# Kernel tuning notes

Hardware: AMD Instinct MI355X
Metric: run time of the kernel (lower is better)

The kernel has to match this reference:

```python
import jax, jax.numpy as jnp
import numpy as np

N, M, D_K, D_V = 8192, 8192, 128, 128
SCALING = 1.0 / D_K  # module uses 1/d_k, NOT 1/sqrt(d_k)


def setup_inputs() -> dict:
    key = jax.random.key(0)
    kq, kk, kv = jax.random.split(key, 3)
    Q = jax.random.normal(kq, (N, D_K), dtype=jnp.float32)
    K = jax.random.normal(kk, (M, D_K), dtype=jnp.float32)
    V = jax.random.normal(kv, (M, D_V), dtype=jnp.float32)
    return {"Q": Q, "K": K, "V": V}


def reference(Q, K, V):
    # dots = Q @ K^T * (1/d_k)  -> [N, M]
    dots = jnp.einsum("nd,md->nm", Q, K) * SCALING
    # softmax over keys; dropout p=0 is identity
    attn = jax.nn.softmax(dots, axis=-1)
    # output = attn @ V -> [N, d_v]
    return jnp.einsum("nm,mv->nv", attn, V)
```

## Files before the change

kernel.cpp:

```cpp
#include <hip/hip_runtime.h>
#include <hip/hip_bf16.h>
#include <cstdint>
#include <cstddef>


typedef __attribute__((ext_vector_type(8))) short short8;
typedef __attribute__((ext_vector_type(4))) short shortx4;
typedef __attribute__((ext_vector_type(4))) float floatx4;
typedef __attribute__((ext_vector_type(16))) float floatx16;
typedef __attribute__((ext_vector_type(8))) _Float16 half8;

#define N_Q    8192
#define N_KV   8192
#define DHEAD  128
#define NSPLIT 8
#define BK     64
#define QSCALE (1.4426950408889634f / 128.0f)

static __device__ __forceinline__ unsigned short f2bf(float x) {
  __hip_bfloat16 h = __float2bfloat16(x);
  unsigned short u;
  __builtin_memcpy(&u, &h, 2);
  return u;
}

static __device__ __forceinline__ uint32_t pack_bf2(float a, float b) {
  return (uint32_t)f2bf(a) | ((uint32_t)f2bf(b) << 16);
}

#define MFMA32(a, b, c) __builtin_amdgcn_mfma_f32_32x32x16_bf16((a), (b), (c), 0, 0, 0)

#define GLD_LDS16(g, l)                                                        \
  __builtin_amdgcn_global_load_lds(                                            \
      (const __attribute__((address_space(1))) void*)(g),                      \
      (__attribute__((address_space(3))) void*)(l), 16, 0, 0)

__global__ void cvt_kernel(const float* __restrict__ K,
                           const float* __restrict__ V,
                           unsigned short* __restrict__ Kbc,
                           unsigned short* __restrict__ Vtc) {
  int bid = blockIdx.x;
  if (bid < 512) {
    int tid = bid * 256 + threadIdx.x;
    int ki = tid & 63;
    int ch = (tid >> 6) & 15;
    int b  = tid >> 10;
    const float* src = K + ((size_t)(b * 64 + ki) * DHEAD + ch * 8);
    floatx4 f0 = *(const floatx4*)src;
    floatx4 f1 = *(const floatx4*)(src + 4);
    short8 o;
    o[0] = (short)f2bf(f0[0]); o[1] = (short)f2bf(f0[1]);
    o[2] = (short)f2bf(f0[2]); o[3] = (short)f2bf(f0[3]);
    o[4] = (short)f2bf(f1[0]); o[5] = (short)f2bf(f1[1]);
    o[6] = (short)f2bf(f1[2]); o[7] = (short)f2bf(f1[3]);
    *(short8*)(Kbc + (size_t)tid * 8) = o;
  } else {
    int tid = (bid - 512) * 256 + threadIdx.x;
    int kh = tid & 1;
    int dv = (tid >> 1) & 127;
    int c2 = (tid >> 8) & 7;
    int b  = tid >> 11;
    int k0 = b * 64 + c2 * 8 + kh * 4;
    shortx4 o;
    o[0] = (short)f2bf(V[(size_t)(k0 + 0) * DHEAD + dv]);
    o[1] = (short)f2bf(V[(size_t)(k0 + 1) * DHEAD + dv]);
    o[2] = (short)f2bf(V[(size_t)(k0 + 2) * DHEAD + dv]);
    o[3] = (short)f2bf(V[(size_t)(k0 + 3) * DHEAD + dv]);
    *(shortx4*)(Vtc + (size_t)tid * 4) = o;
  }
}

__global__ __launch_bounds__(256, 2) void attn_kernel(
    const float* __restrict__ Q, const unsigned short* __restrict__ Kbc,
    const unsigned short* __restrict__ Vtc, _Float16* __restrict__ Opart,
    float* __restrict__ Lst) {
  __shared__ unsigned short lds[8192 + 8192 + 4 * 2048];
  unsigned short* Ks  = lds;
  unsigned short* Vts = lds + 8192;
  unsigned short* Pa  = lds + 16384 + (threadIdx.x >> 6) * 2048;

  const int t = threadIdx.x;
  const int w = t >> 6;
  const int lane = t & 63;
  const int h = lane >> 5;
  const int c = lane & 31;
  const int qbase = blockIdx.x * 128 + w * 32;
  const int sp = blockIdx.y;

  short8 qf[8];
  {
    const float* qrow = Q + (size_t)(qbase + c) * DHEAD + h * 8;
#pragma unroll
    for (int dc = 0; dc < 8; ++dc) {
      floatx4 f0 = *(const floatx4*)(qrow + dc * 16);
      floatx4 f1 = *(const floatx4*)(qrow + dc * 16 + 4);
      short8 s;
      s[0] = (short)f2bf(f0[0] * QSCALE); s[1] = (short)f2bf(f0[1] * QSCALE);
      s[2] = (short)f2bf(f0[2] * QSCALE); s[3] = (short)f2bf(f0[3] * QSCALE);
      s[4] = (short)f2bf(f1[0] * QSCALE); s[5] = (short)f2bf(f1[1] * QSCALE);
      s[6] = (short)f2bf(f1[2] * QSCALE); s[7] = (short)f2bf(f1[3] * QSCALE);
      qf[dc] = s;
    }
  }

  floatx16 acc[4];
#pragma unroll
  for (int i = 0; i < 4; ++i)
#pragma unroll
    for (int r = 0; r < 16; ++r) acc[i][r] = 0.f;
  float lsum = 0.f;

  const int NT = N_KV / NSPLIT / BK;
  const int kb0 = sp * NT;

  for (int it = 0; it < NT; ++it) {
    const int kb = kb0 + it;
    {
      const unsigned short* kg = Kbc + (size_t)kb * 8192;
      const unsigned short* vg = Vtc + (size_t)kb * 8192;
#pragma unroll
      for (int i = 0; i < 4; ++i) {
        int slab = w * 4 + i;
        GLD_LDS16(kg + slab * 512 + lane * 8, Ks + slab * 512);
        GLD_LDS16(vg + slab * 512 + lane * 8, Vts + slab * 512);
      }
    }
    __syncthreads();

    const short8* KsF = (const short8*)Ks;
    uint32_t* pa32 = (uint32_t*)Pa;
#pragma unroll
    for (int st = 0; st < 2; ++st) {
      floatx16 sc;
#pragma unroll
      for (int r = 0; r < 16; ++r) sc[r] = 0.f;
#pragma unroll
      for (int dc = 0; dc < 8; ++dc) {
        short8 a = KsF[(dc * 2 + h) * 64 + st * 32 + c];
        sc = MFMA32(a, qf[dc], sc);
      }
#pragma unroll
      for (int r2 = 0; r2 < 4; ++r2) {
        float p0 = exp2f(sc[r2 * 4 + 0]);
        float p1 = exp2f(sc[r2 * 4 + 1]);
        float p2 = exp2f(sc[r2 * 4 + 2]);
        float p3 = exp2f(sc[r2 * 4 + 3]);
        lsum += (p0 + p1) + (p2 + p3);
        int di = ((st * 4 + r2) * 32 + c) * 4 + h * 2;
        pa32[di + 0] = pack_bf2(p0, p1);
        pa32[di + 1] = pack_bf2(p2, p3);
      }
    }

    const short8* PaF = (const short8*)Pa;
    const short8* VtsF = (const short8*)Vts;
#pragma unroll
    for (int kc = 0; kc < 4; ++kc) {
      short8 pf = PaF[(kc * 2 + h) * 32 + c];
#pragma unroll
      for (int nb = 0; nb < 4; ++nb) {
        short8 bv = VtsF[(kc * 2 + h) * 128 + nb * 32 + c];
        acc[nb] = MFMA32(pf, bv, acc[nb]);
      }
    }
    __syncthreads();
  }

  lsum += __shfl_xor(lsum, 32, 64);
  if (h == 0) Lst[(size_t)sp * N_Q + qbase + c] = lsum;
  _Float16* op = Opart + ((size_t)sp * N_Q + qbase) * DHEAD;
#pragma unroll
  for (int nb = 0; nb < 4; ++nb)
#pragma unroll
    for (int r = 0; r < 16; ++r) {
      int row = (r & 3) + 8 * (r >> 2) + 4 * h;
      op[(size_t)row * DHEAD + nb * 32 + c] = (_Float16)acc[nb][r];
    }
}

__global__ void merge_kernel(const _Float16* __restrict__ Opart,
                             const float* __restrict__ Lst,
                             float* __restrict__ out) {
  int tid = blockIdx.x * blockDim.x + threadIdx.x;
  int g = tid >> 4;
  int d0 = (tid & 15) * 8;
  float den = 0.f;
  float num[8] = {0.f, 0.f, 0.f, 0.f, 0.f, 0.f, 0.f, 0.f};
#pragma unroll
  for (int s = 0; s < NSPLIT; ++s) {
    den += Lst[(size_t)s * N_Q + g];
    half8 o = *(const half8*)(Opart + ((size_t)s * N_Q + g) * DHEAD + d0);
#pragma unroll
    for (int j = 0; j < 8; ++j) num[j] += (float)o[j];
  }
  float inv = 1.0f / den;
  floatx4 r0 = (floatx4){num[0] * inv, num[1] * inv, num[2] * inv, num[3] * inv};
  floatx4 r1 = (floatx4){num[4] * inv, num[5] * inv, num[6] * inv, num[7] * inv};
  float* dst = out + (size_t)g * DHEAD + d0;
  *(floatx4*)dst = r0;
  *(floatx4*)(dst + 4) = r1;
}

extern "C" void kernel_launch(void* const* d_in, const int* in_sizes, int n_in,
                              void* d_out, int out_size, void* d_ws,
                              size_t ws_size, hipStream_t stream) {
  const float* Q = (const float*)d_in[0];
  const float* K = (const float*)d_in[1];
  const float* V = (const float*)d_in[2];
  float* out = (float*)d_out;

  char* ws = (char*)d_ws;
  unsigned short* Kbc = (unsigned short*)(ws);
  unsigned short* Vtc = (unsigned short*)(ws + (2u << 20));
  _Float16* Opart = (_Float16*)(ws + (4u << 20));
  float* Lst = (float*)(ws + (20u << 20));

  cvt_kernel<<<dim3(1536), dim3(256), 0, stream>>>(K, V, Kbc, Vtc);
  attn_kernel<<<dim3(N_Q / 128, NSPLIT), dim3(256), 0, stream>>>(Q, Kbc, Vtc,
                                                                 Opart, Lst);
  merge_kernel<<<dim3(512), dim3(256), 0, stream>>>(Opart, Lst, out);
}
```

Before: 114.9 us.

## Double-buffer V in LDS, read K from global, keep P in registers

Drops the K tile and the per-wave P staging buffer from shared memory. K fragments are now read straight from global memory (L2), and V tiles are double-buffered in LDS with the next tile prefetched while the current one is used. The softmax probabilities are rearranged into the MFMA A-operand layout with lane shuffles instead of an LDS round trip. Occupancy is raised to 3 blocks per CU, and the KV split count goes to 16 when the workspace is large enough. In exchange, K loads now come from global memory with higher latency, and the merge kernel has twice as many partial results to combine.

Measured after the change: 156.3 us. 1.36x slower.

```diff
diff --git a/kernel.cpp b/kernel.cpp
--- a/kernel.cpp
+++ b/kernel.cpp
@@ -13,7 +13,6 @@
 #define N_Q    8192
 #define N_KV   8192
 #define DHEAD  128
-#define NSPLIT 8
 #define BK     64
 #define QSCALE (1.4426950408889634f / 128.0f)
 
@@ -70,14 +69,11 @@
   }
 }
 
-__global__ __launch_bounds__(256, 2) void attn_kernel(
+__global__ __launch_bounds__(256, 3) void attn_kernel(
     const float* __restrict__ Q, const unsigned short* __restrict__ Kbc,
     const unsigned short* __restrict__ Vtc, _Float16* __restrict__ Opart,
     float* __restrict__ Lst) {
-  __shared__ unsigned short lds[8192 + 8192 + 4 * 2048];
-  unsigned short* Ks  = lds;
-  unsigned short* Vts = lds + 8192;
-  unsigned short* Pa  = lds + 16384 + (threadIdx.x >> 6) * 2048;
+  __shared__ unsigned short Vts[2][8192];
 
   const int t = threadIdx.x;
   const int w = t >> 6;
@@ -86,6 +82,9 @@
   const int c = lane & 31;
   const int qbase = blockIdx.x * 128 + w * 32;
   const int sp = blockIdx.y;
+  const int nsp = gridDim.y;
+  const int NT = (N_KV / BK) / nsp;
+  const int kb0 = sp * NT;
 
   short8 qf[8];
   {
@@ -110,25 +109,31 @@
     for (int r = 0; r < 16; ++r) acc[i][r] = 0.f;
   float lsum = 0.f;
 
-  const int NT = N_KV / NSPLIT / BK;
-  const int kb0 = sp * NT;
+  {
+    const unsigned short* vg = Vtc + (size_t)kb0 * 8192;
+#pragma unroll
+    for (int i = 0; i < 4; ++i) {
+      int slab = w * 4 + i;
+      GLD_LDS16(vg + slab * 512 + lane * 8, &Vts[0][0] + slab * 512);
+    }
+  }
+  __syncthreads();
 
   for (int it = 0; it < NT; ++it) {
     const int kb = kb0 + it;
-    {
-      const unsigned short* kg = Kbc + (size_t)kb * 8192;
-      const unsigned short* vg = Vtc + (size_t)kb * 8192;
+    if (it + 1 < NT) {
+      const unsigned short* vg = Vtc + (size_t)(kb + 1) * 8192;
+      unsigned short* dst = &Vts[(it + 1) & 1][0];
 #pragma unroll
       for (int i = 0; i < 4; ++i) {
         int slab = w * 4 + i;
-        GLD_LDS16(kg + slab * 512 + lane * 8, Ks + slab * 512);
-        GLD_LDS16(vg + slab * 512 + lane * 8, Vts + slab * 512);
-      }
-    }
-    __syncthreads();
-
-    const short8* KsF = (const short8*)Ks;
-    uint32_t* pa32 = (uint32_t*)Pa;
+        GLD_LDS16(vg + slab * 512 + lane * 8, dst + slab * 512);
+      }
+    }
+
+    const short8* Kg = (const short8*)(Kbc + (size_t)kb * 8192);
+    const short8* VtsF = (const short8*)&Vts[it & 1][0];
+
 #pragma unroll
     for (int st = 0; st < 2; ++st) {
       floatx16 sc;
@@ -136,9 +141,10 @@
       for (int r = 0; r < 16; ++r) sc[r] = 0.f;
 #pragma unroll
       for (int dc = 0; dc < 8; ++dc) {
-        short8 a = KsF[(dc * 2 + h) * 64 + st * 32 + c];
+        short8 a = Kg[(dc * 2 + h) * 64 + st * 32 + c];
         sc = MFMA32(a, qf[dc], sc);
       }
+      uint32_t qd[8];
 #pragma unroll
       for (int r2 = 0; r2 < 4; ++r2) {
         float p0 = exp2f(sc[r2 * 4 + 0]);
@@ -146,21 +152,30 @@
         float p2 = exp2f(sc[r2 * 4 + 2]);
         float p3 = exp2f(sc[r2 * 4 + 3]);
         lsum += (p0 + p1) + (p2 + p3);
-        int di = ((st * 4 + r2) * 32 + c) * 4 + h * 2;
-        pa32[di + 0] = pack_bf2(p0, p1);
-        pa32[di + 1] = pack_bf2(p2, p3);
-      }
-    }
-
-    const short8* PaF = (const short8*)Pa;
-    const short8* VtsF = (const short8*)Vts;
-#pragma unroll
-    for (int kc = 0; kc < 4; ++kc) {
-      short8 pf = PaF[(kc * 2 + h) * 32 + c];
-#pragma unroll
-      for (int nb = 0; nb < 4; ++nb) {
-        short8 bv = VtsF[(kc * 2 + h) * 128 + nb * 32 + c];
-        acc[nb] = MFMA32(pf, bv, acc[nb]);
+        qd[r2 * 2 + 0] = pack_bf2(p0, p1);
+        qd[r2 * 2 + 1] = pack_bf2(p2, p3);
+      }
+#pragma unroll
+      for (int b = 0; b < 2; ++b) {
+        uint32_t s0 = h ? qd[(2 * b) * 2 + 0] : qd[(2 * b + 1) * 2 + 0];
+        uint32_t s1 = h ? qd[(2 * b) * 2 + 1] : qd[(2 * b + 1) * 2 + 1];
+        uint32_t r0 = __shfl_xor(s0, 32, 64);
+        uint32_t r1 = __shfl_xor(s1, 32, 64);
+        uint32_t o0 = h ? qd[(2 * b + 1) * 2 + 0] : qd[(2 * b) * 2 + 0];
+        uint32_t o1 = h ? qd[(2 * b + 1) * 2 + 1] : qd[(2 * b) * 2 + 1];
+        uint32_t f[4];
+        f[0] = h ? r0 : o0;
+        f[1] = h ? r1 : o1;
+        f[2] = h ? o0 : r0;
+        f[3] = h ? o1 : r1;
+        short8 pf;
+        __builtin_memcpy(&pf, f, 16);
+        const int kc = st * 2 + b;
+#pragma unroll
+        for (int nb = 0; nb < 4; ++nb) {
+          short8 bv = VtsF[(kc * 2 + h) * 128 + nb * 32 + c];
+          acc[nb] = MFMA32(pf, bv, acc[nb]);
+        }
       }
     }
     __syncthreads();
@@ -180,14 +195,13 @@
 
 __global__ void merge_kernel(const _Float16* __restrict__ Opart,
                              const float* __restrict__ Lst,
-                             float* __restrict__ out) {
+                             float* __restrict__ out, int nsp) {
   int tid = blockIdx.x * blockDim.x + threadIdx.x;
   int g = tid >> 4;
   int d0 = (tid & 15) * 8;
   float den = 0.f;
   float num[8] = {0.f, 0.f, 0.f, 0.f, 0.f, 0.f, 0.f, 0.f};
-#pragma unroll
-  for (int s = 0; s < NSPLIT; ++s) {
+  for (int s = 0; s < nsp; ++s) {
     den += Lst[(size_t)s * N_Q + g];
     half8 o = *(const half8*)(Opart + ((size_t)s * N_Q + g) * DHEAD + d0);
 #pragma unroll
@@ -209,14 +223,17 @@
   const float* V = (const float*)d_in[2];
   float* out = (float*)d_out;
 
+  const size_t need16 = (4ull << 20) + 16ull * N_Q * DHEAD * 2 + 16ull * N_Q * 4;
+  const int nsp = (ws_size >= need16) ? 16 : 8;
+
   char* ws = (char*)d_ws;
   unsigned short* Kbc = (unsigned short*)(ws);
   unsigned short* Vtc = (unsigned short*)(ws + (2u << 20));
   _Float16* Opart = (_Float16*)(ws + (4u << 20));
-  float* Lst = (float*)(ws + (20u << 20));
+  float* Lst = (float*)(ws + (4ull << 20) + (size_t)nsp * N_Q * DHEAD * 2);
 
   cvt_kernel<<<dim3(1536), dim3(256), 0, stream>>>(K, V, Kbc, Vtc);
-  attn_kernel<<<dim3(N_Q / 128, NSPLIT), dim3(256), 0, stream>>>(Q, Kbc, Vtc,
-                                                                 Opart, Lst);
-  merge_kernel<<<dim3(512), dim3(256), 0, stream>>>(Opart, Lst, out);
-}
+  attn_kernel<<<dim3(N_Q / 128, nsp), dim3(256), 0, stream>>>(Q, Kbc, Vtc,
+                                                              Opart, Lst);
+  merge_kernel<<<dim3(512), dim3(256), 0, stream>>>(Opart, Lst, out, nsp);
+}
```
